# Optimization experiments

Measured on AMD Instinct MI355X. Metric: run time of the kernel, lower is better.

## Reference

```python
import jax, jax.numpy as jnp
import numpy as np

N_NODES = 50000
N_EDGES = 640000
N_FEAT = 512
HIDDEN = 128
N_CLASSES = 64


def setup_inputs() -> dict:
    key = jax.random.key(0)
    k1, k2, k3, k4, k5, k6 = jax.random.split(key, 6)
    x = jax.random.normal(k1, (N_NODES, N_FEAT), dtype=jnp.float32)
    edge_index = jax.random.randint(k2, (2, N_EDGES), 0, N_NODES, dtype=jnp.int32)
    # GCNConv weights (glorot-ish scale) and biases
    W1 = jax.random.normal(k3, (N_FEAT, HIDDEN), dtype=jnp.float32) / np.sqrt(N_FEAT)
    b1 = jnp.zeros((HIDDEN,), dtype=jnp.float32)
    W2 = jax.random.normal(k4, (HIDDEN, N_CLASSES), dtype=jnp.float32) / np.sqrt(HIDDEN)
    b2 = jnp.zeros((N_CLASSES,), dtype=jnp.float32)
    return {"x": x, "edge_index": edge_index, "W1": W1, "b1": b1, "W2": W2, "b2": b2}


def reference(x, edge_index, W1, b1, W2, b2):
    N = x.shape[0]
    # Add self-loops (PyG GCNConv default)
    loop = jnp.arange(N, dtype=edge_index.dtype)
    src = jnp.concatenate([edge_index[0], loop])
    dst = jnp.concatenate([edge_index[1], loop])
    # Symmetric normalization: deg computed over targets incl. self-loops
    deg = jax.ops.segment_sum(jnp.ones(src.shape[0], dtype=x.dtype), dst, num_segments=N)
    dinv = jax.lax.rsqrt(deg)  # deg >= 1 thanks to self-loops
    norm = dinv[src] * dinv[dst]  # [E+N]

    def gcn_conv(h, W, b):
        h = h @ W                          # dense transform first (smaller msg dim)
        msg = h[src] * norm[:, None]       # gather + normalize
        return jax.ops.segment_sum(msg, dst, num_segments=N) + b  # scatter-add + bias

    h = jax.nn.relu(gcn_conv(x, W1, b1))
    # F.dropout with training=False is identity (eval mode)
    return gcn_conv(h, W2, b2)
```

## Files before the change

kernel.cpp:

```cpp
#include <hip/hip_runtime.h>


#define NNODES 50000
#define NEDGES 640000
#define NFEAT 512
#define NHID 128
#define NCLS 64

typedef _Float16 f16x8 __attribute__((ext_vector_type(8)));
typedef float f32x4 __attribute__((ext_vector_type(4)));

__global__ void k_zero2(int* __restrict__ a, int* __restrict__ b, int n) {
  int i = blockIdx.x * blockDim.x + threadIdx.x;
  if (i < n) { a[i] = 0; b[i] = 0; }
}

__global__ void k_hist(const int* __restrict__ dst, int* __restrict__ indeg, int E) {
  int i = blockIdx.x * blockDim.x + threadIdx.x;
  if (i < E) atomicAdd(&indeg[dst[i]], 1);
}

__global__ void k_dinv(const int* __restrict__ indeg, float* __restrict__ dinv, int n) {
  int i = blockIdx.x * blockDim.x + threadIdx.x;
  if (i < n) dinv[i] = 1.0f / sqrtf((float)(indeg[i] + 1));
}

__global__ void k_scan_block(const int* __restrict__ indeg, int* __restrict__ row_start,
                             int* __restrict__ blocksum, int n) {
  __shared__ int sdata[256];
  int t = threadIdx.x;
  int base = blockIdx.x * 1024 + t * 4;
  int v[4];
#pragma unroll
  for (int j = 0; j < 4; ++j) v[j] = (base + j < n) ? indeg[base + j] : 0;
  int tsum = v[0] + v[1] + v[2] + v[3];
  sdata[t] = tsum;
  __syncthreads();
  for (int off = 1; off < 256; off <<= 1) {
    int x = (t >= off) ? sdata[t - off] : 0;
    __syncthreads();
    sdata[t] += x;
    __syncthreads();
  }
  int excl = sdata[t] - tsum;
  if (t == 255) blocksum[blockIdx.x] = sdata[255];
  int run = excl;
#pragma unroll
  for (int j = 0; j < 4; ++j) {
    if (base + j < n) { row_start[base + j] = run; run += v[j]; }
  }
}

__global__ void k_scan_top(const int* __restrict__ blocksum, int* __restrict__ blockoff, int nb) {
  if (threadIdx.x == 0 && blockIdx.x == 0) {
    int run = 0;
    for (int i = 0; i < nb; ++i) { blockoff[i] = run; run += blocksum[i]; }
  }
}

__global__ void k_scan_add(int* __restrict__ row_start, const int* __restrict__ blockoff,
                           int n, int E) {
  int i = blockIdx.x * blockDim.x + threadIdx.x;
  if (i < n) row_start[i] += blockoff[i >> 10];
  if (i == 0) row_start[n] = E;
}

__global__ void k_scatter(const int* __restrict__ src, const int* __restrict__ dst,
                          const int* __restrict__ row_start, int* __restrict__ cursor,
                          const float* __restrict__ dinv, int* __restrict__ csr_src,
                          float* __restrict__ csr_norm, int E) {
  int e = blockIdx.x * blockDim.x + threadIdx.x;
  if (e < E) {
    int s = src[e], d = dst[e];
    int pos = atomicAdd(&cursor[d], 1);
    int idx = row_start[d] + pos;
    csr_src[idx] = s;
    csr_norm[idx] = dinv[s] * dinv[d];
  }
}

__global__ void k_wcvt(const float* __restrict__ W, _Float16* __restrict__ Wt_hi,
                       _Float16* __restrict__ Wt_lo, int K, int Nc) {
  int i = blockIdx.x * blockDim.x + threadIdx.x;
  if (i < K * Nc) {
    int k = i / Nc, n = i % Nc;
    float v = W[i];
    _Float16 h = (_Float16)v;
    Wt_hi[(size_t)n * K + k] = h;
    Wt_lo[(size_t)n * K + k] = (_Float16)((v - (float)h) * 1024.0f);
  }
}

template <int K, int WY, int WX, bool AFP32>
__global__ __launch_bounds__(256) void k_mfma_gemm(
    const float* __restrict__ A32, const _Float16* __restrict__ Ahi,
    const _Float16* __restrict__ Alo, const _Float16* __restrict__ Bhi,
    const _Float16* __restrict__ Blo, float* __restrict__ C, int M, int N) {
  const int wid = threadIdx.x >> 6;
  const int lane = threadIdx.x & 63;
  const int wy = wid / WX, wx = wid % WX;
  const int r0 = (blockIdx.x * WY + wy) * 64;
  const int c0 = (blockIdx.y * WX + wx) * 64;
  const int lrow = lane & 15;
  const int koff = (lane >> 4) * 8;

  f32x4 acc_h[4][4] = {};
  f32x4 acc_l[4][4] = {};

  for (int k0 = 0; k0 < K; k0 += 32) {
    f16x8 bh[4], bl[4];
#pragma unroll
    for (int cf = 0; cf < 4; ++cf) {
      size_t boff = (size_t)(c0 + cf * 16 + lrow) * K + k0 + koff;
      bh[cf] = *(const f16x8*)(Bhi + boff);
      bl[cf] = *(const f16x8*)(Blo + boff);
    }
#pragma unroll
    for (int rf = 0; rf < 4; ++rf) {
      int row = r0 + rf * 16 + lrow;
      row = row < M ? row : M - 1;
      f16x8 ah, al;
      if (AFP32) {
        const float* ap = A32 + (size_t)row * K + k0 + koff;
        float4 v0 = *(const float4*)ap;
        float4 v1 = *(const float4*)(ap + 4);
        float vv[8] = {v0.x, v0.y, v0.z, v0.w, v1.x, v1.y, v1.z, v1.w};
#pragma unroll
        for (int j = 0; j < 8; ++j) {
          _Float16 h = (_Float16)vv[j];
          ah[j] = h;
          al[j] = (_Float16)((vv[j] - (float)h) * 1024.0f);
        }
      } else {
        size_t aoff = (size_t)row * K + k0 + koff;
        ah = *(const f16x8*)(Ahi + aoff);
        al = *(const f16x8*)(Alo + aoff);
      }
#pragma unroll
      for (int cf = 0; cf < 4; ++cf) {
        acc_h[rf][cf] =
            __builtin_amdgcn_mfma_f32_16x16x32_f16(ah, bh[cf], acc_h[rf][cf], 0, 0, 0);
        acc_l[rf][cf] =
            __builtin_amdgcn_mfma_f32_16x16x32_f16(ah, bl[cf], acc_l[rf][cf], 0, 0, 0);
        acc_l[rf][cf] =
            __builtin_amdgcn_mfma_f32_16x16x32_f16(al, bh[cf], acc_l[rf][cf], 0, 0, 0);
      }
    }
  }

#pragma unroll
  for (int rf = 0; rf < 4; ++rf) {
    if (r0 + rf * 16 >= M) continue;
    int rbase = r0 + rf * 16 + (lane >> 4) * 4;
#pragma unroll
    for (int cf = 0; cf < 4; ++cf) {
      int col = c0 + cf * 16 + lrow;
#pragma unroll
      for (int q = 0; q < 4; ++q) {
        C[(size_t)(rbase + q) * N + col] =
            acc_h[rf][cf][q] + acc_l[rf][cf][q] * (1.0f / 1024.0f);
      }
    }
  }
}

template <int F, bool RELU, bool EMIT16>
__global__ __launch_bounds__(F) void k_agg(const float* __restrict__ h,
                                           const float* __restrict__ bias,
                                           const int* __restrict__ row_start,
                                           const int* __restrict__ csr_src,
                                           const float* __restrict__ csr_norm,
                                           const float* __restrict__ dinv,
                                           float* __restrict__ out,
                                           _Float16* __restrict__ out_hi,
                                           _Float16* __restrict__ out_lo) {
  int n = blockIdx.x;
  int f = threadIdx.x;
  float dn = dinv[n];
  float acc0 = dn * dn * h[(size_t)n * F + f] + bias[f];
  float acc1 = 0.f, acc2 = 0.f, acc3 = 0.f;
  int e0 = row_start[n], e1 = row_start[n + 1];
  int e = e0;
  for (; e + 4 <= e1; e += 4) {
    int s0 = csr_src[e + 0]; float w0 = csr_norm[e + 0];
    int s1 = csr_src[e + 1]; float w1 = csr_norm[e + 1];
    int s2 = csr_src[e + 2]; float w2 = csr_norm[e + 2];
    int s3 = csr_src[e + 3]; float w3 = csr_norm[e + 3];
    acc0 += w0 * h[(size_t)s0 * F + f];
    acc1 += w1 * h[(size_t)s1 * F + f];
    acc2 += w2 * h[(size_t)s2 * F + f];
    acc3 += w3 * h[(size_t)s3 * F + f];
  }
  for (; e < e1; ++e) {
    int s = csr_src[e];
    acc0 += csr_norm[e] * h[(size_t)s * F + f];
  }
  float acc = (acc0 + acc1) + (acc2 + acc3);
  if (RELU) acc = fmaxf(acc, 0.f);
  if (EMIT16) {
    _Float16 hh = (_Float16)acc;
    out_hi[(size_t)n * F + f] = hh;
    out_lo[(size_t)n * F + f] = (_Float16)((acc - (float)hh) * 1024.0f);
  } else {
    out[(size_t)n * F + f] = acc;
  }
}

static inline size_t align256(size_t x) { return (x + 255) & ~(size_t)255; }

extern "C" void kernel_launch(void* const* d_in, const int* in_sizes, int n_in,
                              void* d_out, int out_size, void* d_ws, size_t ws_size,
                              hipStream_t stream) {
  const float* x = (const float*)d_in[0];
  const int* edge = (const int*)d_in[1];
  const float* W1 = (const float*)d_in[2];
  const float* b1 = (const float*)d_in[3];
  const float* W2 = (const float*)d_in[4];
  const float* b2 = (const float*)d_in[5];
  float* out = (float*)d_out;

  const int N = NNODES;
  const int E = NEDGES;
  const int* src = edge;
  const int* dst = edge + E;

  char* w = (char*)d_ws;
  int* indeg = (int*)w;          w += align256((size_t)N * 4);
  int* cursor = (int*)w;         w += align256((size_t)N * 4);
  float* dinv = (float*)w;       w += align256((size_t)N * 4);
  int* row_start = (int*)w;      w += align256((size_t)(N + 1) * 4);
  int* blocksum = (int*)w;       w += align256(64 * 4);
  int* blockoff = (int*)w;       w += align256(64 * 4);
  int* csr_src = (int*)w;        w += align256((size_t)E * 4);
  float* csr_norm = (float*)w;   w += align256((size_t)E * 4);
  _Float16* W1t_hi = (_Float16*)w; w += align256((size_t)NFEAT * NHID * 2);
  _Float16* W1t_lo = (_Float16*)w; w += align256((size_t)NFEAT * NHID * 2);
  _Float16* W2t_hi = (_Float16*)w; w += align256((size_t)NHID * NCLS * 2);
  _Float16* W2t_lo = (_Float16*)w; w += align256((size_t)NHID * NCLS * 2);
  float* h0 = (float*)w;         w += align256((size_t)N * NHID * 4);
  _Float16* h1_hi = (_Float16*)w; w += align256((size_t)N * NHID * 2);
  _Float16* h1_lo = (_Float16*)w; w += align256((size_t)N * NHID * 2);
  float* h2 = (float*)w;         w += align256((size_t)N * NCLS * 4);

  const int nblk_n = (N + 255) / 256;
  const int nblk_e = (E + 255) / 256;
  const int nblk_scan = (N + 1023) / 1024;

  k_zero2<<<nblk_n, 256, 0, stream>>>(indeg, cursor, N);
  k_hist<<<nblk_e, 256, 0, stream>>>(dst, indeg, E);
  k_dinv<<<nblk_n, 256, 0, stream>>>(indeg, dinv, N);
  k_scan_block<<<nblk_scan, 256, 0, stream>>>(indeg, row_start, blocksum, N);
  k_scan_top<<<1, 64, 0, stream>>>(blocksum, blockoff, nblk_scan);
  k_scan_add<<<nblk_n, 256, 0, stream>>>(row_start, blockoff, N, E);
  k_scatter<<<nblk_e, 256, 0, stream>>>(src, dst, row_start, cursor, dinv,
                                        csr_src, csr_norm, E);

  k_wcvt<<<(NFEAT * NHID + 255) / 256, 256, 0, stream>>>(W1, W1t_hi, W1t_lo,
                                                         NFEAT, NHID);
  k_wcvt<<<(NHID * NCLS + 255) / 256, 256, 0, stream>>>(W2, W2t_hi, W2t_lo,
                                                        NHID, NCLS);

  {
    dim3 grid((N + 127) / 128, 1);
    k_mfma_gemm<NFEAT, 2, 2, true><<<grid, 256, 0, stream>>>(
        x, nullptr, nullptr, W1t_hi, W1t_lo, h0, N, NHID);
  }
  k_agg<NHID, true, true><<<N, NHID, 0, stream>>>(h0, b1, row_start, csr_src,
                                                  csr_norm, dinv, nullptr,
                                                  h1_hi, h1_lo);
  {
    dim3 grid((N + 255) / 256, 1);
    k_mfma_gemm<NHID, 4, 1, false><<<grid, 256, 0, stream>>>(
        nullptr, h1_hi, h1_lo, W2t_hi, W2t_lo, h2, N, NCLS);
  }
  k_agg<NCLS, false, false><<<N, NCLS, 0, stream>>>(h2, b2, row_start, csr_src,
                                                    csr_norm, dinv, out,
                                                    nullptr, nullptr);
}
```

Baseline: 410.9 us.

## Pad CSR rows to multiples of four, double-buffer GEMMs, wave-per-node aggregation

CSR rows are padded to a multiple of four with zero-weight self entries, so the aggregation loops need no scalar tail. Both GEMMs are specialised with smaller per-wave tiles and register double-buffering of the A/B fragments to overlap loads with MFMA. Aggregation now uses one 64-lane wave per node, with float2 vector loads for the 128-wide layer and eight independent accumulators for more memory-level parallelism. This costs an extra padding kernel and a larger CSR buffer, and the smaller tiles cut reuse of the B operand.

Measured after the change: 416.1 us. No clear change (+1.3%).

```diff
diff --git a/kernel.cpp b/kernel.cpp
--- a/kernel.cpp
+++ b/kernel.cpp
@@ -8,6 +8,7 @@
 #define NCLS 64
 
 typedef _Float16 f16x8 __attribute__((ext_vector_type(8)));
+typedef _Float16 f16x2 __attribute__((ext_vector_type(2)));
 typedef float f32x4 __attribute__((ext_vector_type(4)));
 
 __global__ void k_zero2(int* __restrict__ a, int* __restrict__ b, int n) {
@@ -32,7 +33,11 @@
   int base = blockIdx.x * 1024 + t * 4;
   int v[4];
 #pragma unroll
-  for (int j = 0; j < 4; ++j) v[j] = (base + j < n) ? indeg[base + j] : 0;
+  for (int j = 0; j < 4; ++j) {
+    int idx = base + j;
+    int d = (idx < n) ? indeg[idx] : 0;
+    v[j] = (d + 3) & ~3;
+  }
   int tsum = v[0] + v[1] + v[2] + v[3];
   sdata[t] = tsum;
   __syncthreads();
@@ -47,7 +52,7 @@
   int run = excl;
 #pragma unroll
   for (int j = 0; j < 4; ++j) {
-    if (base + j < n) { row_start[base + j] = run; run += v[j]; }
+    if (base + j <= n) { row_start[base + j] = run; run += v[j]; }
   }
 }
 
@@ -58,11 +63,20 @@
   }
 }
 
-__global__ void k_scan_add(int* __restrict__ row_start, const int* __restrict__ blockoff,
-                           int n, int E) {
-  int i = blockIdx.x * blockDim.x + threadIdx.x;
-  if (i < n) row_start[i] += blockoff[i >> 10];
-  if (i == 0) row_start[n] = E;
+__global__ void k_scan_add(int* __restrict__ row_start, const int* __restrict__ blockoff, int n) {
+  int i = blockIdx.x * blockDim.x + threadIdx.x;
+  if (i <= n) row_start[i] += blockoff[i >> 10];
+}
+
+__global__ void k_pad(const int* __restrict__ indeg, const int* __restrict__ row_start,
+                      int* __restrict__ csr_src, float* __restrict__ csr_norm, int n) {
+  int i = blockIdx.x * blockDim.x + threadIdx.x;
+  if (i < n) {
+    int d = indeg[i];
+    int p = (d + 3) & ~3;
+    int b = row_start[i];
+    for (int j = d; j < p; ++j) { csr_src[b + j] = i; csr_norm[b + j] = 0.f; }
+  }
 }
 
 __global__ void k_scatter(const int* __restrict__ src, const int* __restrict__ dst,
@@ -91,119 +105,214 @@
   }
 }
 
-template <int K, int WY, int WX, bool AFP32>
-__global__ __launch_bounds__(256) void k_mfma_gemm(
-    const float* __restrict__ A32, const _Float16* __restrict__ Ahi,
-    const _Float16* __restrict__ Alo, const _Float16* __restrict__ Bhi,
-    const _Float16* __restrict__ Blo, float* __restrict__ C, int M, int N) {
-  const int wid = threadIdx.x >> 6;
-  const int lane = threadIdx.x & 63;
-  const int wy = wid / WX, wx = wid % WX;
-  const int r0 = (blockIdx.x * WY + wy) * 64;
-  const int c0 = (blockIdx.y * WX + wx) * 64;
-  const int lrow = lane & 15;
-  const int koff = (lane >> 4) * 8;
-
-  f32x4 acc_h[4][4] = {};
-  f32x4 acc_l[4][4] = {};
-
-  for (int k0 = 0; k0 < K; k0 += 32) {
-    f16x8 bh[4], bl[4];
-#pragma unroll
-    for (int cf = 0; cf < 4; ++cf) {
-      size_t boff = (size_t)(c0 + cf * 16 + lrow) * K + k0 + koff;
-      bh[cf] = *(const f16x8*)(Bhi + boff);
-      bl[cf] = *(const f16x8*)(Blo + boff);
-    }
-#pragma unroll
-    for (int rf = 0; rf < 4; ++rf) {
+__global__ __launch_bounds__(256) void k_gemm1(const float* __restrict__ A,
+                                               const _Float16* __restrict__ Bhi,
+                                               const _Float16* __restrict__ Blo,
+                                               float* __restrict__ C, int M) {
+  constexpr int K = NFEAT, N = NHID;
+  const int wid = threadIdx.x >> 6, lane = threadIdx.x & 63;
+  const int wy = wid >> 1, wx = wid & 1;
+  const int r0 = blockIdx.x * 64 + wy * 32;
+  const int c0 = wx * 64;
+  const int lrow = lane & 15, koff = (lane >> 4) * 8;
+
+  f32x4 acc_h[2][4] = {};
+  f32x4 acc_l[2][4] = {};
+  f16x8 bh[2][4], bl[2][4], ah[2][2], al[2][2];
+
+  auto loadB = [&](int buf, int k0) {
+#pragma unroll
+    for (int cf = 0; cf < 4; ++cf) {
+      size_t off = (size_t)(c0 + cf * 16 + lrow) * K + k0 + koff;
+      bh[buf][cf] = *(const f16x8*)(Bhi + off);
+      bl[buf][cf] = *(const f16x8*)(Blo + off);
+    }
+  };
+  auto loadA = [&](int buf, int k0) {
+#pragma unroll
+    for (int rf = 0; rf < 2; ++rf) {
       int row = r0 + rf * 16 + lrow;
       row = row < M ? row : M - 1;
-      f16x8 ah, al;
-      if (AFP32) {
-        const float* ap = A32 + (size_t)row * K + k0 + koff;
-        float4 v0 = *(const float4*)ap;
-        float4 v1 = *(const float4*)(ap + 4);
-        float vv[8] = {v0.x, v0.y, v0.z, v0.w, v1.x, v1.y, v1.z, v1.w};
-#pragma unroll
-        for (int j = 0; j < 8; ++j) {
-          _Float16 h = (_Float16)vv[j];
-          ah[j] = h;
-          al[j] = (_Float16)((vv[j] - (float)h) * 1024.0f);
-        }
-      } else {
-        size_t aoff = (size_t)row * K + k0 + koff;
-        ah = *(const f16x8*)(Ahi + aoff);
-        al = *(const f16x8*)(Alo + aoff);
+      const float* p = A + (size_t)row * K + k0 + koff;
+      float4 v0 = *(const float4*)p;
+      float4 v1 = *(const float4*)(p + 4);
+      float vv[8] = {v0.x, v0.y, v0.z, v0.w, v1.x, v1.y, v1.z, v1.w};
+#pragma unroll
+      for (int j = 0; j < 8; ++j) {
+        _Float16 h = (_Float16)vv[j];
+        ah[buf][rf][j] = h;
+        al[buf][rf][j] = (_Float16)((vv[j] - (float)h) * 1024.0f);
       }
+    }
+  };
+
+  loadB(0, 0);
+  loadA(0, 0);
+#pragma unroll
+  for (int ks = 0; ks < K / 32; ++ks) {
+    const int cur = ks & 1, nxt = cur ^ 1;
+    if (ks + 1 < K / 32) { loadB(nxt, (ks + 1) * 32); loadA(nxt, (ks + 1) * 32); }
+#pragma unroll
+    for (int rf = 0; rf < 2; ++rf)
 #pragma unroll
       for (int cf = 0; cf < 4; ++cf) {
-        acc_h[rf][cf] =
-            __builtin_amdgcn_mfma_f32_16x16x32_f16(ah, bh[cf], acc_h[rf][cf], 0, 0, 0);
-        acc_l[rf][cf] =
-            __builtin_amdgcn_mfma_f32_16x16x32_f16(ah, bl[cf], acc_l[rf][cf], 0, 0, 0);
-        acc_l[rf][cf] =
-            __builtin_amdgcn_mfma_f32_16x16x32_f16(al, bh[cf], acc_l[rf][cf], 0, 0, 0);
+        acc_h[rf][cf] = __builtin_amdgcn_mfma_f32_16x16x32_f16(ah[cur][rf], bh[cur][cf],
+                                                               acc_h[rf][cf], 0, 0, 0);
+        acc_l[rf][cf] = __builtin_amdgcn_mfma_f32_16x16x32_f16(ah[cur][rf], bl[cur][cf],
+                                                               acc_l[rf][cf], 0, 0, 0);
+        acc_l[rf][cf] = __builtin_amdgcn_mfma_f32_16x16x32_f16(al[cur][rf], bh[cur][cf],
+                                                               acc_l[rf][cf], 0, 0, 0);
       }
-    }
-  }
-
-#pragma unroll
-  for (int rf = 0; rf < 4; ++rf) {
+  }
+
+#pragma unroll
+  for (int rf = 0; rf < 2; ++rf) {
     if (r0 + rf * 16 >= M) continue;
     int rbase = r0 + rf * 16 + (lane >> 4) * 4;
 #pragma unroll
     for (int cf = 0; cf < 4; ++cf) {
       int col = c0 + cf * 16 + lrow;
 #pragma unroll
-      for (int q = 0; q < 4; ++q) {
+      for (int q = 0; q < 4; ++q)
         C[(size_t)(rbase + q) * N + col] =
             acc_h[rf][cf][q] + acc_l[rf][cf][q] * (1.0f / 1024.0f);
-      }
-    }
-  }
-}
-
-template <int F, bool RELU, bool EMIT16>
-__global__ __launch_bounds__(F) void k_agg(const float* __restrict__ h,
-                                           const float* __restrict__ bias,
-                                           const int* __restrict__ row_start,
-                                           const int* __restrict__ csr_src,
-                                           const float* __restrict__ csr_norm,
-                                           const float* __restrict__ dinv,
-                                           float* __restrict__ out,
-                                           _Float16* __restrict__ out_hi,
-                                           _Float16* __restrict__ out_lo) {
-  int n = blockIdx.x;
-  int f = threadIdx.x;
-  float dn = dinv[n];
-  float acc0 = dn * dn * h[(size_t)n * F + f] + bias[f];
-  float acc1 = 0.f, acc2 = 0.f, acc3 = 0.f;
-  int e0 = row_start[n], e1 = row_start[n + 1];
-  int e = e0;
-  for (; e + 4 <= e1; e += 4) {
-    int s0 = csr_src[e + 0]; float w0 = csr_norm[e + 0];
-    int s1 = csr_src[e + 1]; float w1 = csr_norm[e + 1];
-    int s2 = csr_src[e + 2]; float w2 = csr_norm[e + 2];
-    int s3 = csr_src[e + 3]; float w3 = csr_norm[e + 3];
-    acc0 += w0 * h[(size_t)s0 * F + f];
-    acc1 += w1 * h[(size_t)s1 * F + f];
-    acc2 += w2 * h[(size_t)s2 * F + f];
-    acc3 += w3 * h[(size_t)s3 * F + f];
-  }
-  for (; e < e1; ++e) {
-    int s = csr_src[e];
-    acc0 += csr_norm[e] * h[(size_t)s * F + f];
-  }
-  float acc = (acc0 + acc1) + (acc2 + acc3);
-  if (RELU) acc = fmaxf(acc, 0.f);
+    }
+  }
+}
+
+__global__ __launch_bounds__(256) void k_gemm2(const _Float16* __restrict__ Ahi,
+                                               const _Float16* __restrict__ Alo,
+                                               const _Float16* __restrict__ Bhi,
+                                               const _Float16* __restrict__ Blo,
+                                               float* __restrict__ C, int M) {
+  constexpr int K = NHID, N = NCLS;
+  const int wid = threadIdx.x >> 6, lane = threadIdx.x & 63;
+  const int r0 = blockIdx.x * 64 + wid * 16;
+  const int lrow = lane & 15, koff = (lane >> 4) * 8;
+
+  f32x4 acc_h[4] = {};
+  f32x4 acc_l[4] = {};
+  f16x8 bh[2][4], bl[2][4], ah[2], al[2];
+
+  auto loadB = [&](int buf, int k0) {
+#pragma unroll
+    for (int cf = 0; cf < 4; ++cf) {
+      size_t off = (size_t)(cf * 16 + lrow) * K + k0 + koff;
+      bh[buf][cf] = *(const f16x8*)(Bhi + off);
+      bl[buf][cf] = *(const f16x8*)(Blo + off);
+    }
+  };
+  auto loadA = [&](int buf, int k0) {
+    int row = r0 + lrow;
+    row = row < M ? row : M - 1;
+    size_t off = (size_t)row * K + k0 + koff;
+    ah[buf] = *(const f16x8*)(Ahi + off);
+    al[buf] = *(const f16x8*)(Alo + off);
+  };
+
+  loadB(0, 0);
+  loadA(0, 0);
+#pragma unroll
+  for (int ks = 0; ks < K / 32; ++ks) {
+    const int cur = ks & 1, nxt = cur ^ 1;
+    if (ks + 1 < K / 32) { loadB(nxt, (ks + 1) * 32); loadA(nxt, (ks + 1) * 32); }
+#pragma unroll
+    for (int cf = 0; cf < 4; ++cf) {
+      acc_h[cf] = __builtin_amdgcn_mfma_f32_16x16x32_f16(ah[cur], bh[cur][cf],
+                                                         acc_h[cf], 0, 0, 0);
+      acc_l[cf] = __builtin_amdgcn_mfma_f32_16x16x32_f16(ah[cur], bl[cur][cf],
+                                                         acc_l[cf], 0, 0, 0);
+      acc_l[cf] = __builtin_amdgcn_mfma_f32_16x16x32_f16(al[cur], bh[cur][cf],
+                                                         acc_l[cf], 0, 0, 0);
+    }
+  }
+
+  if (r0 < M) {
+    int rbase = r0 + (lane >> 4) * 4;
+#pragma unroll
+    for (int cf = 0; cf < 4; ++cf) {
+      int col = cf * 16 + lrow;
+#pragma unroll
+      for (int q = 0; q < 4; ++q)
+        C[(size_t)(rbase + q) * N + col] = acc_h[cf][q] + acc_l[cf][q] * (1.0f / 1024.0f);
+    }
+  }
+}
+
+template <bool RELU, bool EMIT16>
+__global__ __launch_bounds__(256) void k_agg128(
+    const float* __restrict__ h, const float* __restrict__ bias,
+    const int* __restrict__ row_start, const int* __restrict__ csr_src,
+    const float* __restrict__ csr_norm, const float* __restrict__ dinv,
+    float* __restrict__ out, _Float16* __restrict__ out_hi,
+    _Float16* __restrict__ out_lo, int N) {
+  int node = blockIdx.x * 4 + (threadIdx.x >> 6);
+  if (node >= N) return;
+  int lane = threadIdx.x & 63;
+  const float2* hp = (const float2*)h;
+
+  float dn = dinv[node];
+  float2 bs = ((const float2*)bias)[lane];
+  float2 sf = hp[(size_t)node * 64 + lane];
+  float2 a0 = {dn * dn * sf.x + bs.x, dn * dn * sf.y + bs.y};
+  float2 a1 = {0.f, 0.f}, a2 = {0.f, 0.f}, a3 = {0.f, 0.f};
+  float2 a4 = {0.f, 0.f}, a5 = {0.f, 0.f}, a6 = {0.f, 0.f}, a7 = {0.f, 0.f};
+
+  int e = row_start[node], e1 = row_start[node + 1];
+#define GATH(ACC, EI)                                        \
+  {                                                          \
+    int s_ = csr_src[EI];                                    \
+    float w_ = csr_norm[EI];                                 \
+    float2 v_ = hp[(size_t)s_ * 64 + lane];                  \
+    ACC.x += w_ * v_.x;                                      \
+    ACC.y += w_ * v_.y;                                      \
+  }
+  for (; e + 8 <= e1; e += 8) {
+    GATH(a0, e + 0) GATH(a1, e + 1) GATH(a2, e + 2) GATH(a3, e + 3)
+    GATH(a4, e + 4) GATH(a5, e + 5) GATH(a6, e + 6) GATH(a7, e + 7)
+  }
+  if (e < e1) {
+    GATH(a0, e + 0) GATH(a1, e + 1) GATH(a2, e + 2) GATH(a3, e + 3)
+  }
+#undef GATH
+  float ax = ((a0.x + a1.x) + (a2.x + a3.x)) + ((a4.x + a5.x) + (a6.x + a7.x));
+  float ay = ((a0.y + a1.y) + (a2.y + a3.y)) + ((a4.y + a5.y) + (a6.y + a7.y));
+  if (RELU) { ax = fmaxf(ax, 0.f); ay = fmaxf(ay, 0.f); }
   if (EMIT16) {
-    _Float16 hh = (_Float16)acc;
-    out_hi[(size_t)n * F + f] = hh;
-    out_lo[(size_t)n * F + f] = (_Float16)((acc - (float)hh) * 1024.0f);
+    _Float16 hx = (_Float16)ax, hy = (_Float16)ay;
+    f16x2 vh = {hx, hy};
+    f16x2 vl = {(_Float16)((ax - (float)hx) * 1024.0f),
+                (_Float16)((ay - (float)hy) * 1024.0f)};
+    *(f16x2*)(out_hi + (size_t)node * 128 + lane * 2) = vh;
+    *(f16x2*)(out_lo + (size_t)node * 128 + lane * 2) = vl;
   } else {
-    out[(size_t)n * F + f] = acc;
-  }
+    ((float2*)out)[(size_t)node * 64 + lane] = {ax, ay};
+  }
+}
+
+__global__ __launch_bounds__(256) void k_agg64(
+    const float* __restrict__ h, const float* __restrict__ bias,
+    const int* __restrict__ row_start, const int* __restrict__ csr_src,
+    const float* __restrict__ csr_norm, const float* __restrict__ dinv,
+    float* __restrict__ out, int N) {
+  int node = blockIdx.x * 4 + (threadIdx.x >> 6);
+  if (node >= N) return;
+  int f = threadIdx.x & 63;
+  float dn = dinv[node];
+  float a0 = dn * dn * h[(size_t)node * 64 + f] + bias[f];
+  float a1 = 0.f, a2 = 0.f, a3 = 0.f, a4 = 0.f, a5 = 0.f, a6 = 0.f, a7 = 0.f;
+  int e = row_start[node], e1 = row_start[node + 1];
+#define GATH(ACC, EI) ACC += csr_norm[EI] * h[(size_t)csr_src[EI] * 64 + f];
+  for (; e + 8 <= e1; e += 8) {
+    GATH(a0, e + 0) GATH(a1, e + 1) GATH(a2, e + 2) GATH(a3, e + 3)
+    GATH(a4, e + 4) GATH(a5, e + 5) GATH(a6, e + 6) GATH(a7, e + 7)
+  }
+  if (e < e1) {
+    GATH(a0, e + 0) GATH(a1, e + 1) GATH(a2, e + 2) GATH(a3, e + 3)
+  }
+#undef GATH
+  out[(size_t)node * 64 + f] =
+      ((a0 + a1) + (a2 + a3)) + ((a4 + a5) + (a6 + a7));
 }
 
 static inline size_t align256(size_t x) { return (x + 255) & ~(size_t)255; }
@@ -221,37 +330,40 @@
 
   const int N = NNODES;
   const int E = NEDGES;
+  const int EPAD = E + 3 * N + 256;
   const int* src = edge;
   const int* dst = edge + E;
 
   char* w = (char*)d_ws;
-  int* indeg = (int*)w;          w += align256((size_t)N * 4);
-  int* cursor = (int*)w;         w += align256((size_t)N * 4);
-  float* dinv = (float*)w;       w += align256((size_t)N * 4);
-  int* row_start = (int*)w;      w += align256((size_t)(N + 1) * 4);
-  int* blocksum = (int*)w;       w += align256(64 * 4);
-  int* blockoff = (int*)w;       w += align256(64 * 4);
-  int* csr_src = (int*)w;        w += align256((size_t)E * 4);
-  float* csr_norm = (float*)w;   w += align256((size_t)E * 4);
+  int* indeg = (int*)w;            w += align256((size_t)N * 4);
+  int* cursor = (int*)w;           w += align256((size_t)N * 4);
+  float* dinv = (float*)w;         w += align256((size_t)N * 4);
+  int* row_start = (int*)w;        w += align256((size_t)(N + 1) * 4);
+  int* blocksum = (int*)w;         w += align256(64 * 4);
+  int* blockoff = (int*)w;         w += align256(64 * 4);
+  int* csr_src = (int*)w;          w += align256((size_t)EPAD * 4);
+  float* csr_norm = (float*)w;     w += align256((size_t)EPAD * 4);
   _Float16* W1t_hi = (_Float16*)w; w += align256((size_t)NFEAT * NHID * 2);
   _Float16* W1t_lo = (_Float16*)w; w += align256((size_t)NFEAT * NHID * 2);
   _Float16* W2t_hi = (_Float16*)w; w += align256((size_t)NHID * NCLS * 2);
   _Float16* W2t_lo = (_Float16*)w; w += align256((size_t)NHID * NCLS * 2);
-  float* h0 = (float*)w;         w += align256((size_t)N * NHID * 4);
-  _Float16* h1_hi = (_Float16*)w; w += align256((size_t)N * NHID * 2);
-  _Float16* h1_lo = (_Float16*)w; w += align256((size_t)N * NHID * 2);
-  float* h2 = (float*)w;         w += align256((size_t)N * NCLS * 4);
+  float* h0 = (float*)w;           w += align256((size_t)N * NHID * 4);
+  _Float16* h1_hi = (_Float16*)w;  w += align256((size_t)N * NHID * 2);
+  _Float16* h1_lo = (_Float16*)w;  w += align256((size_t)N * NHID * 2);
+  float* h2 = (float*)w;           w += align256((size_t)N * NCLS * 4);
 
   const int nblk_n = (N + 255) / 256;
+  const int nblk_n1 = (N + 1 + 255) / 256;
   const int nblk_e = (E + 255) / 256;
-  const int nblk_scan = (N + 1023) / 1024;
+  const int nblk_scan = (N + 1 + 1023) / 1024;
 
   k_zero2<<<nblk_n, 256, 0, stream>>>(indeg, cursor, N);
   k_hist<<<nblk_e, 256, 0, stream>>>(dst, indeg, E);
   k_dinv<<<nblk_n, 256, 0, stream>>>(indeg, dinv, N);
   k_scan_block<<<nblk_scan, 256, 0, stream>>>(indeg, row_start, blocksum, N);
   k_scan_top<<<1, 64, 0, stream>>>(blocksum, blockoff, nblk_scan);
-  k_scan_add<<<nblk_n, 256, 0, stream>>>(row_start, blockoff, N, E);
+  k_scan_add<<<nblk_n1, 256, 0, stream>>>(row_start, blockoff, N);
+  k_pad<<<nblk_n, 256, 0, stream>>>(indeg, row_start, csr_src, csr_norm, N);
   k_scatter<<<nblk_e, 256, 0, stream>>>(src, dst, row_start, cursor, dinv,
                                         csr_src, csr_norm, E);
 
@@ -260,20 +372,10 @@
   k_wcvt<<<(NHID * NCLS + 255) / 256, 256, 0, stream>>>(W2, W2t_hi, W2t_lo,
                                                         NHID, NCLS);
 
-  {
-    dim3 grid((N + 127) / 128, 1);
-    k_mfma_gemm<NFEAT, 2, 2, true><<<grid, 256, 0, stream>>>(
-        x, nullptr, nullptr, W1t_hi, W1t_lo, h0, N, NHID);
-  }
-  k_agg<NHID, true, true><<<N, NHID, 0, stream>>>(h0, b1, row_start, csr_src,
-                                                  csr_norm, dinv, nullptr,
-                                                  h1_hi, h1_lo);
-  {
-    dim3 grid((N + 255) / 256, 1);
-    k_mfma_gemm<NHID, 4, 1, false><<<grid, 256, 0, stream>>>(
-        nullptr, h1_hi, h1_lo, W2t_hi, W2t_lo, h2, N, NCLS);
-  }
-  k_agg<NCLS, false, false><<<N, NCLS, 0, stream>>>(h2, b2, row_start, csr_src,
-                                                    csr_norm, dinv, out,
-                                                    nullptr, nullptr);
-}
+  k_gemm1<<<(N + 63) / 64, 256, 0, stream>>>(x, W1t_hi, W1t_lo, h0, N);
+  k_agg128<true, true><<<(N + 3) / 4, 256, 0, stream>>>(
+      h0, b1, row_start, csr_src, csr_norm, dinv, nullptr, h1_hi, h1_lo, N);
+  k_gemm2<<<(N + 63) / 64, 256, 0, stream>>>(h1_hi, h1_lo, W2t_hi, W2t_lo, h2, N);
+  k_agg64<<<(N + 3) / 4, 256, 0, stream>>>(h2, b2, row_start, csr_src, csr_norm,
+                                           dinv, out, N);
+}
```
